# Optimization experiments

Measured on AMD Instinct MI355X. Metric: run time of the kernel, lower is better.

## Reference

```python
import jax, jax.numpy as jnp
import numpy as np

N = 100000
E = 500000
HID = 256
N_EDGE_TYPES = 5
N_ATOM = 16
N_CHARGE = 7
NUM_RBF = 16
CUTOFF = 5.0
LN_EPS = 1e-5


def _xavier(key, shape):
    fan_in, fan_out = shape[0], shape[1]
    lim = float(np.sqrt(6.0 / (fan_in + fan_out)))
    return jax.random.uniform(key, shape, jnp.float32, -lim, lim)


def setup_inputs() -> dict:
    key = jax.random.key(0)
    ks = jax.random.split(key, 12)
    input_dim = HID * 2 + NUM_RBF + N_ATOM + N_CHARGE  # 551
    h = jax.random.normal(ks[0], (N, HID), jnp.float32)
    x = jax.random.normal(ks[1], (N, 3), jnp.float32)
    spawn_node_idx = jax.random.randint(ks[2], (E,), 0, N)
    existing_node_idx = jax.random.randint(ks[3], (E,), 0, N)
    ins_x = jax.random.normal(ks[4], (E, 3), jnp.float32)
    ins_a = jax.random.randint(ks[5], (E,), 0, N_ATOM)
    ins_c = jax.random.randint(ks[6], (E,), 0, N_CHARGE)
    # MLP params (Xavier weights, zero biases; LayerNorm gamma=1, beta=0)
    W1 = _xavier(ks[7], (input_dim, HID)); b1 = jnp.zeros((HID,), jnp.float32)
    g1 = jnp.ones((HID,), jnp.float32); be1 = jnp.zeros((HID,), jnp.float32)
    W2 = _xavier(ks[8], (HID, HID // 2)); b2 = jnp.zeros((HID // 2,), jnp.float32)
    g2 = jnp.ones((HID // 2,), jnp.float32); be2 = jnp.zeros((HID // 2,), jnp.float32)
    W3 = _xavier(ks[9], (HID // 2, N_EDGE_TYPES)); b3 = jnp.zeros((N_EDGE_TYPES,), jnp.float32)
    # Gaussian RBF parameters: centers on [0, cutoff], shared width from spacing
    rbf_mu = jnp.linspace(0.0, CUTOFF, NUM_RBF).astype(jnp.float32)
    delta = CUTOFF / (NUM_RBF - 1)
    rbf_gamma = jnp.asarray(1.0 / (2.0 * delta * delta), jnp.float32)
    return {"h": h, "x": x, "spawn_node_idx": spawn_node_idx,
            "existing_node_idx": existing_node_idx, "ins_x": ins_x,
            "ins_a": ins_a, "ins_c": ins_c,
            "W1": W1, "b1": b1, "g1": g1, "be1": be1,
            "W2": W2, "b2": b2, "g2": g2, "be2": be2,
            "W3": W3, "b3": b3, "rbf_mu": rbf_mu, "rbf_gamma": rbf_gamma}


def _layer_norm(z, gamma, beta):
    mu = jnp.mean(z, axis=-1, keepdims=True)
    var = jnp.mean((z - mu) ** 2, axis=-1, keepdims=True)
    return (z - mu) * jax.lax.rsqrt(var + LN_EPS) * gamma + beta


def reference(h, x, spawn_node_idx, existing_node_idx, ins_x, ins_a, ins_c,
              W1, b1, g1, be1, W2, b2, g2, be2, W3, b3, rbf_mu, rbf_gamma):
    # gather node pairs  [E, HID] / [E, 3]
    h_spawn = h[spawn_node_idx]
    h_existing = h[existing_node_idx]
    existing_pos = x[existing_node_idx]
    # distance + Gaussian RBF  [E, NUM_RBF]
    d = jnp.maximum(jnp.linalg.norm(ins_x - existing_pos, axis=-1), 1e-6)
    dist_features = jnp.exp(-rbf_gamma * (d[:, None] - rbf_mu) ** 2)
    # one-hot insertion type features
    ins_atom = jax.nn.one_hot(ins_a, N_ATOM, dtype=h.dtype)
    ins_charge = jax.nn.one_hot(ins_c, N_CHARGE, dtype=h.dtype)
    feats = jnp.concatenate([h_spawn, h_existing, dist_features, ins_atom, ins_charge], axis=-1)
    # 3-layer MLP: Linear -> LN -> SiLU -> Linear -> LN -> SiLU -> Linear
    z = jax.nn.silu(_layer_norm(feats @ W1 + b1, g1, be1))
    z = jax.nn.silu(_layer_norm(z @ W2 + b2, g2, be2))
    return z @ W3 + b3  # [E, N_EDGE_TYPES]
```

## Files before the change

### kernel.cpp

```cpp
#include <hip/hip_runtime.h>
#include <stdint.h>

#define NN 100000
#define EE 500000
#define HIDD 256
#define LN_EPS 1e-5f

typedef _Float16 half8 __attribute__((ext_vector_type(8)));
typedef _Float16 half4 __attribute__((ext_vector_type(4)));
typedef __fp16 fp16x2 __attribute__((ext_vector_type(2)));
typedef float f32x4 __attribute__((ext_vector_type(4)));

#define LBAR() asm volatile("s_waitcnt lgkmcnt(0)\n\ts_barrier" ::: "memory")

__device__ __forceinline__ unsigned short f2h(float f) {
  _Float16 h = (_Float16)f;
  union { _Float16 hh; unsigned short us; } u; u.hh = h;
  return u.us;
}

__device__ __forceinline__ unsigned pkrtz(float a, float b) {
  union { fp16x2 h; unsigned u; } c;
  c.h = __builtin_amdgcn_cvt_pkrtz(a, b);
  return c.u;
}

__device__ __forceinline__ float fast_silu(float y) {
  float e = __expf(-y);
  return y * __builtin_amdgcn_rcpf(1.f + e);
}

__device__ __forceinline__ half8 ldg8(const unsigned short* p) {
  return *(const half8*)p;
}

__global__ __launch_bounds__(256) void prep_kern(const float* __restrict__ h,
                                                 const float* __restrict__ W1,
                                                 const float* __restrict__ W2,
                                                 const float* __restrict__ W3,
                                                 unsigned short* __restrict__ hb,
                                                 unsigned short* __restrict__ w1sw,
                                                 unsigned short* __restrict__ w2sw,
                                                 unsigned short* __restrict__ w3sw) {
  int b = blockIdx.x;
  if (b < 712) {
    int t = b * 256 + threadIdx.x;
    if (t < 147456) {
      int chunk = t >> 14, rem = t & 16383;
      int kq = rem >> 11, n = (rem >> 3) & 255, j = rem & 7;
      int k = (chunk << 6) + (kq << 3) + j;
      float v = (k < 551) ? W1[k * 256 + n] : 0.f;
      w1sw[t] = f2h(v);
    } else if (t < 147456 + 32768) {
      int t2 = t - 147456;
      int chunk = t2 >> 13, rem = t2 & 8191;
      int kq = rem >> 10, n = (rem >> 3) & 127, j = rem & 7;
      int k = (chunk << 6) + (kq << 3) + j;
      w2sw[t2] = f2h(W2[k * 128 + n]);
    } else if (t < 147456 + 32768 + 2048) {
      int t3 = t - 180224;
      int kq = t3 >> 7, o = (t3 >> 3) & 15, j = t3 & 7;
      int k = (kq << 3) + j;
      w3sw[t3] = f2h((o < 5) ? W3[k * 5 + o] : 0.f);
    }
  } else {
    int i = ((b - 712) * 256 + threadIdx.x) * 8;
    float4 v0 = *(const float4*)(h + i);
    float4 v1 = *(const float4*)(h + i + 4);
    uint4 u;
    u.x = pkrtz(v0.x, v0.y); u.y = pkrtz(v0.z, v0.w);
    u.z = pkrtz(v1.x, v1.y); u.w = pkrtz(v1.z, v1.w);
    *(uint4*)(hb + i) = u;
  }
}

struct __align__(16) SMem {
  short r1[16384];
  float red[512];
  _Float16 b1h[256], g1h[256], be1h[256];
  _Float16 b2h[128], g2h[128], be2h[128];
  float muv[16];
  float b3v[8];
  int spI[64], exI[64];
};

__global__ __launch_bounds__(256, 3)
void edge_head_main(const float* __restrict__ h, const float* __restrict__ x,
                    const int* __restrict__ spawn, const int* __restrict__ exist,
                    const float* __restrict__ insx, const int* __restrict__ insa,
                    const int* __restrict__ insc,
                    const float* __restrict__ b1, const float* __restrict__ g1,
                    const float* __restrict__ be1,
                    const float* __restrict__ b2, const float* __restrict__ g2,
                    const float* __restrict__ be2,
                    const float* __restrict__ b3, const float* __restrict__ mu,
                    const float* __restrict__ gammaP,
                    const unsigned short* __restrict__ w1sw,
                    const unsigned short* __restrict__ w2sw,
                    const unsigned short* __restrict__ w3swg,
                    const unsigned short* __restrict__ hb, int use_hb,
                    float* __restrict__ out) {
  __shared__ SMem sm;
  const int t = threadIdx.x;
  const int base = blockIdx.x * 64;
  const int lane = t & 63;
  const int wv = t >> 6;
  const int cl = lane & 15;
  const int q = lane >> 4;
  const int sx = (cl & 7) << 3;

  sm.b1h[t] = (_Float16)b1[t]; sm.g1h[t] = (_Float16)g1[t]; sm.be1h[t] = (_Float16)be1[t];
  if (t < 128) { sm.b2h[t] = (_Float16)b2[t]; sm.g2h[t] = (_Float16)g2[t]; sm.be2h[t] = (_Float16)be2[t]; }
  if (t < 16) sm.muv[t] = mu[t];
  if (t < 8) sm.b3v[t] = (t < 5) ? b3[t] : 0.f;
  if (t < 64) {
    int e = base + t; int ec = e < EE ? e : EE - 1;
    sm.spI[t] = spawn[ec]; sm.exI[t] = exist[ec];
  }
  const float gma = gammaP[0];

  LBAR();

  int4 f8a = {0,0,0,0}, f8b = {0,0,0,0};
  int k1 = 16, k2 = 32;
  if (t < 64) {
    int e = base + t; int ec = e < EE ? e : EE - 1;
    float ix0 = insx[ec * 3], ix1 = insx[ec * 3 + 1], ix2 = insx[ec * 3 + 2];
    int nd = sm.exI[t];
    float dx = ix0 - x[nd * 3], dy = ix1 - x[nd * 3 + 1], dz = ix2 - x[nd * 3 + 2];
    float d = fmaxf(sqrtf(dx * dx + dy * dy + dz * dz), 1e-6f);
    k1 = 16 + insa[ec]; k2 = 32 + insc[ec];
    float rb[16];
#pragma unroll
    for (int k = 0; k < 16; ++k) { float dd = d - sm.muv[k]; rb[k] = __expf(-gma * dd * dd); }
    uint4 ua, ub;
    ua.x = pkrtz(rb[0], rb[1]);  ua.y = pkrtz(rb[2], rb[3]);
    ua.z = pkrtz(rb[4], rb[5]);  ua.w = pkrtz(rb[6], rb[7]);
    ub.x = pkrtz(rb[8], rb[9]);  ub.y = pkrtz(rb[10], rb[11]);
    ub.z = pkrtz(rb[12], rb[13]); ub.w = pkrtz(rb[14], rb[15]);
    f8a = *(int4*)&ua; f8b = *(int4*)&ub;
  }

  const int row0 = t >> 3, p0 = t & 7;
  const int row1 = row0 + 32;
  const int sw0 = ((p0 ^ (row0 & 7)) << 3);
  const int sw1 = ((p0 ^ (row1 & 7)) << 3);

  int4 pA, pB;
  if (use_hb) {
    pA = *(const int4*)(hb + (size_t)sm.spI[row0] * HIDD + p0 * 8);
    pB = *(const int4*)(hb + (size_t)sm.spI[row1] * HIDD + p0 * 8);
  } else {
    const float* sA = h + (size_t)sm.spI[row0] * HIDD + p0 * 8;
    const float* sB = h + (size_t)sm.spI[row1] * HIDD + p0 * 8;
    float4 a0 = *(const float4*)sA, a1 = *(const float4*)(sA + 4);
    float4 b0 = *(const float4*)sB, b1v_ = *(const float4*)(sB + 4);
    uint4 ua, ub;
    ua.x = pkrtz(a0.x, a0.y); ua.y = pkrtz(a0.z, a0.w); ua.z = pkrtz(a1.x, a1.y); ua.w = pkrtz(a1.z, a1.w);
    ub.x = pkrtz(b0.x, b0.y); ub.y = pkrtz(b0.z, b0.w); ub.z = pkrtz(b1v_.x, b1v_.y); ub.w = pkrtz(b1v_.z, b1v_.w);
    pA = *(int4*)&ua; pB = *(int4*)&ub;
  }
  *(int4*)&sm.r1[row0 * 64 + sw0] = pA;
  *(int4*)&sm.r1[row1 * 64 + sw1] = pB;
  if (use_hb) {
    pA = *(const int4*)(hb + (size_t)sm.spI[row0] * HIDD + 64 + p0 * 8);
    pB = *(const int4*)(hb + (size_t)sm.spI[row1] * HIDD + 64 + p0 * 8);
  } else {
    const float* sA = h + (size_t)sm.spI[row0] * HIDD + 64 + p0 * 8;
    const float* sB = h + (size_t)sm.spI[row1] * HIDD + 64 + p0 * 8;
    float4 a0 = *(const float4*)sA, a1 = *(const float4*)(sA + 4);
    float4 b0 = *(const float4*)sB, b1v_ = *(const float4*)(sB + 4);
    uint4 ua, ub;
    ua.x = pkrtz(a0.x, a0.y); ua.y = pkrtz(a0.z, a0.w); ua.z = pkrtz(a1.x, a1.y); ua.w = pkrtz(a1.z, a1.w);
    ub.x = pkrtz(b0.x, b0.y); ub.y = pkrtz(b0.z, b0.w); ub.z = pkrtz(b1v_.x, b1v_.y); ub.w = pkrtz(b1v_.z, b1v_.w);
    pA = *(int4*)&ua; pB = *(int4*)&ub;
  }

  const unsigned short* w1p = w1sw + q * 2048 + wv * 512 + cl * 8;
  half8 fcur[8], fnext[8];
#pragma unroll
  for (int ks = 0; ks < 2; ++ks)
#pragma unroll
    for (int i = 0; i < 4; ++i)
      fcur[ks * 4 + i] = ldg8(w1p + ks * 8192 + i * 128);

  LBAR();

  f32x4 acc[4][4];
#pragma unroll
  for (int i = 0; i < 4; ++i)
#pragma unroll
    for (int j = 0; j < 4; ++j) acc[i][j] = (f32x4){0.f, 0.f, 0.f, 0.f};

#pragma unroll
  for (int c = 0; c < 9; ++c) {
    if (c < 7) {
      const int nb = ((c + 1) & 1) * 4096;
      *(int4*)&sm.r1[nb + row0 * 64 + sw0] = pA;
      *(int4*)&sm.r1[nb + row1 * 64 + sw1] = pB;
      if (c < 6) {
        const int cn = c + 2;
        const int* sel = (cn < 4) ? sm.spI : sm.exI;
        const int colb = (cn & 3) * 64;
        if (use_hb) {
          pA = *(const int4*)(hb + (size_t)sel[row0] * HIDD + colb + p0 * 8);
          pB = *(const int4*)(hb + (size_t)sel[row1] * HIDD + colb + p0 * 8);
        } else {
          const float* sA = h + (size_t)sel[row0] * HIDD + colb + p0 * 8;
          const float* sB = h + (size_t)sel[row1] * HIDD + colb + p0 * 8;
          float4 a0 = *(const float4*)sA, a1 = *(const float4*)(sA + 4);
          float4 b0 = *(const float4*)sB, b1v_ = *(const float4*)(sB + 4);
          uint4 ua, ub;
          ua.x = pkrtz(a0.x, a0.y); ua.y = pkrtz(a0.z, a0.w); ua.z = pkrtz(a1.x, a1.y); ua.w = pkrtz(a1.z, a1.w);
          ub.x = pkrtz(b0.x, b0.y); ub.y = pkrtz(b0.z, b0.w); ub.z = pkrtz(b1v_.x, b1v_.y); ub.w = pkrtz(b1v_.z, b1v_.w);
          pA = *(int4*)&ua; pB = *(int4*)&ub;
        }
      }
    } else if (c == 7) {
      if (t < 64) {
        short* rp = &sm.r1[t * 64];
        const int sw = t & 7;
#pragma unroll
        for (int g = 0; g < 8; ++g) {
          int4 v = (g == 0) ? f8a : (g == 1) ? f8b : (int4){0, 0, 0, 0};
          *(int4*)&rp[(g ^ sw) * 8] = v;
        }
        rp[((k1 >> 3) ^ sw) * 8 + (k1 & 7)] = (short)0x3C00;
        rp[((k2 >> 3) ^ sw) * 8 + (k2 & 7)] = (short)0x3C00;
      }
    }
    if (c < 8) {
      const unsigned short* wp = w1p + (c + 1) * 16384;
#pragma unroll
      for (int ks = 0; ks < 2; ++ks)
#pragma unroll
        for (int i = 0; i < 4; ++i)
          fnext[ks * 4 + i] = ldg8(wp + ks * 8192 + i * 128);
    }
    const int cb = (c & 1) * 4096;
#pragma unroll
    for (int ks = 0; ks < 2; ++ks) {
      half8 bf[4];
#pragma unroll
      for (int j = 0; j < 4; ++j)
        bf[j] = *(const half8*)&sm.r1[cb + (j * 16 + cl) * 64 + ((ks * 32 + q * 8) ^ sx)];
#pragma unroll
      for (int i = 0; i < 4; ++i)
#pragma unroll
        for (int j = 0; j < 4; ++j)
          acc[i][j] = __builtin_amdgcn_mfma_f32_16x16x32_f16(fcur[ks * 4 + i], bf[j], acc[i][j], 0, 0, 0);
    }
#pragma unroll
    for (int u = 0; u < 8; ++u) fcur[u] = fnext[u];
    LBAR();
  }

  float bf1[4][4];
#pragma unroll
  for (int i = 0; i < 4; ++i) {
    half4 b4 = *(const half4*)&sm.b1h[wv * 64 + i * 16 + q * 4];
#pragma unroll
    for (int r = 0; r < 4; ++r) bf1[i][r] = (float)b4[r];
  }
  float S1arr[4], Q1arr[4];
#pragma unroll
  for (int j = 0; j < 4; ++j) {
    float S = 0.f, Q = 0.f;
#pragma unroll
    for (int i = 0; i < 4; ++i)
#pragma unroll
      for (int r = 0; r < 4; ++r) {
        float v = acc[i][j][r] + bf1[i][r];
        acc[i][j][r] = v; S += v; Q += v * v;
      }
    S += __shfl_xor(S, 16); S += __shfl_xor(S, 32);
    Q += __shfl_xor(Q, 16); Q += __shfl_xor(Q, 32);
    S1arr[j] = S; Q1arr[j] = Q;
  }
  if (q == 0) {
#pragma unroll
    for (int j = 0; j < 4; ++j) {
      sm.red[wv * 64 + j * 16 + cl] = S1arr[j];
      sm.red[256 + wv * 64 + j * 16 + cl] = Q1arr[j];
    }
  }
  LBAR();
  float mean1[4], rstd1[4];
#pragma unroll
  for (int j = 0; j < 4; ++j) {
    int m = j * 16 + cl;
    float S = sm.red[m] + sm.red[64 + m] + sm.red[128 + m] + sm.red[192 + m];
    float Q = sm.red[256 + m] + sm.red[320 + m] + sm.red[384 + m] + sm.red[448 + m];
    float mn = S * (1.f / 256.f);
    mean1[j] = mn;
    rstd1[j] = rsqrtf(Q * (1.f / 256.f) - mn * mn + LN_EPS);
  }
#pragma unroll
  for (int i = 0; i < 4; ++i) {
    half4 g4 = *(const half4*)&sm.g1h[wv * 64 + i * 16 + q * 4];
    half4 e4 = *(const half4*)&sm.be1h[wv * 64 + i * 16 + q * 4];
    float gf[4], ef[4];
#pragma unroll
    for (int r = 0; r < 4; ++r) { gf[r] = (float)g4[r]; ef[r] = (float)e4[r]; }
#pragma unroll
    for (int j = 0; j < 4; ++j) {
      float s0 = fast_silu((acc[i][j][0] - mean1[j]) * rstd1[j] * gf[0] + ef[0]);
      float s1 = fast_silu((acc[i][j][1] - mean1[j]) * rstd1[j] * gf[1] + ef[1]);
      float s2 = fast_silu((acc[i][j][2] - mean1[j]) * rstd1[j] * gf[2] + ef[2]);
      float s3 = fast_silu((acc[i][j][3] - mean1[j]) * rstd1[j] * gf[3] + ef[3]);
      uint2 w; w.x = pkrtz(s0, s1); w.y = pkrtz(s2, s3);
      int m = j * 16 + cl;
      int k0 = wv * 64 + i * 16 + q * 4;
      *(uint2*)&sm.r1[m * 256 + (k0 ^ ((m & 7) << 3))] = w;
    }
  }
  LBAR();

  half8 af3[4];
#pragma unroll
  for (int ks = 0; ks < 4; ++ks)
    af3[ks] = ldg8(w3swg + (ks * 4 + q) * 128 + cl * 8);

  const unsigned short* w2p = w2sw + q * 1024 + wv * 256 + cl * 8;
  f32x4 acc2[2][4];
#pragma unroll
  for (int i = 0; i < 2; ++i)
#pragma unroll
    for (int j = 0; j < 4; ++j) acc2[i][j] = (f32x4){0.f, 0.f, 0.f, 0.f};
#pragma unroll
  for (int c2 = 0; c2 < 4; ++c2) {
#pragma unroll
    for (int ks = 0; ks < 2; ++ks) {
      half8 a0 = ldg8(w2p + c2 * 8192 + ks * 4096);
      half8 a1 = ldg8(w2p + c2 * 8192 + ks * 4096 + 128);
      half8 bf[4];
#pragma unroll
      for (int j = 0; j < 4; ++j)
        bf[j] = *(const half8*)&sm.r1[(j * 16 + cl) * 256 + ((c2 * 64 + ks * 32 + q * 8) ^ sx)];
#pragma unroll
      for (int j = 0; j < 4; ++j) {
        acc2[0][j] = __builtin_amdgcn_mfma_f32_16x16x32_f16(a0, bf[j], acc2[0][j], 0, 0, 0);
        acc2[1][j] = __builtin_amdgcn_mfma_f32_16x16x32_f16(a1, bf[j], acc2[1][j], 0, 0, 0);
      }
    }
  }

  float bf2[2][4];
#pragma unroll
  for (int i = 0; i < 2; ++i) {
    half4 b4 = *(const half4*)&sm.b2h[wv * 32 + i * 16 + q * 4];
#pragma unroll
    for (int r = 0; r < 4; ++r) bf2[i][r] = (float)b4[r];
  }
  float S2arr[4], Q2arr[4];
#pragma unroll
  for (int j = 0; j < 4; ++j) {
    float S = 0.f, Q = 0.f;
#pragma unroll
    for (int i = 0; i < 2; ++i)
#pragma unroll
      for (int r = 0; r < 4; ++r) {
        float v = acc2[i][j][r] + bf2[i][r];
        acc2[i][j][r] = v; S += v; Q += v * v;
      }
    S += __shfl_xor(S, 16); S += __shfl_xor(S, 32);
    Q += __shfl_xor(Q, 16); Q += __shfl_xor(Q, 32);
    S2arr[j] = S; Q2arr[j] = Q;
  }
  if (q == 0) {
#pragma unroll
    for (int j = 0; j < 4; ++j) {
      sm.red[wv * 64 + j * 16 + cl] = S2arr[j];
      sm.red[256 + wv * 64 + j * 16 + cl] = Q2arr[j];
    }
  }
  LBAR();
  float mean2[4], rstd2[4];
#pragma unroll
  for (int j = 0; j < 4; ++j) {
    int m = j * 16 + cl;
    float S = sm.red[m] + sm.red[64 + m] + sm.red[128 + m] + sm.red[192 + m];
    float Q = sm.red[256 + m] + sm.red[320 + m] + sm.red[384 + m] + sm.red[448 + m];
    float mn = S * (1.f / 128.f);
    mean2[j] = mn;
    rstd2[j] = rsqrtf(Q * (1.f / 128.f) - mn * mn + LN_EPS);
  }
#pragma unroll
  for (int i = 0; i < 2; ++i) {
    half4 g4 = *(const half4*)&sm.g2h[wv * 32 + i * 16 + q * 4];
    half4 e4 = *(const half4*)&sm.be2h[wv * 32 + i * 16 + q * 4];
    float gf[4], ef[4];
#pragma unroll
    for (int r = 0; r < 4; ++r) { gf[r] = (float)g4[r]; ef[r] = (float)e4[r]; }
#pragma unroll
    for (int j = 0; j < 4; ++j) {
      float s0 = fast_silu((acc2[i][j][0] - mean2[j]) * rstd2[j] * gf[0] + ef[0]);
      float s1 = fast_silu((acc2[i][j][1] - mean2[j]) * rstd2[j] * gf[1] + ef[1]);
      float s2 = fast_silu((acc2[i][j][2] - mean2[j]) * rstd2[j] * gf[2] + ef[2]);
      float s3 = fast_silu((acc2[i][j][3] - mean2[j]) * rstd2[j] * gf[3] + ef[3]);
      uint2 w; w.x = pkrtz(s0, s1); w.y = pkrtz(s2, s3);
      int m = j * 16 + cl;
      int k0 = wv * 32 + i * 16 + q * 4;
      *(uint2*)&sm.r1[m * 128 + (k0 ^ ((m & 7) << 3))] = w;
    }
  }
  LBAR();

  f32x4 a3 = (f32x4){0.f, 0.f, 0.f, 0.f};
  const int m3 = wv * 16 + cl;
  const int sx3 = (m3 & 7) << 3;
#pragma unroll
  for (int ks = 0; ks < 4; ++ks) {
    half8 bf = *(const half8*)&sm.r1[m3 * 128 + ((ks * 32 + q * 8) ^ sx3)];
    a3 = __builtin_amdgcn_mfma_f32_16x16x32_f16(af3[ks], bf, a3, 0, 0, 0);
  }
  int e = base + m3;
  if (e < EE) {
#pragma unroll
    for (int r = 0; r < 4; ++r) {
      int o = q * 4 + r;
      if (o < 5) out[e * 5 + o] = a3[r] + sm.b3v[o];
    }
  }
}

extern "C" void kernel_launch(void* const* d_in, const int* in_sizes, int n_in,
                              void* d_out, int out_size, void* d_ws, size_t ws_size,
                              hipStream_t stream) {
  const float* h    = (const float*)d_in[0];
  const float* x    = (const float*)d_in[1];
  const int* spawn  = (const int*)d_in[2];
  const int* exist  = (const int*)d_in[3];
  const float* insx = (const float*)d_in[4];
  const int* insa   = (const int*)d_in[5];
  const int* insc   = (const int*)d_in[6];
  const float* W1   = (const float*)d_in[7];
  const float* b1   = (const float*)d_in[8];
  const float* g1   = (const float*)d_in[9];
  const float* be1  = (const float*)d_in[10];
  const float* W2   = (const float*)d_in[11];
  const float* b2   = (const float*)d_in[12];
  const float* g2   = (const float*)d_in[13];
  const float* be2  = (const float*)d_in[14];
  const float* W3   = (const float*)d_in[15];
  const float* b3   = (const float*)d_in[16];
  const float* mu   = (const float*)d_in[17];
  const float* gma  = (const float*)d_in[18];

  unsigned short* w1sw = (unsigned short*)d_ws;
  unsigned short* w2sw = w1sw + 147456;
  unsigned short* w3sw = w2sw + 32768;
  unsigned short* hb   = w3sw + 2048;
  const size_t need_hb = 364544ull + (size_t)NN * HIDD * 2ull;
  int use_hb = (ws_size >= need_hb) ? 1 : 0;

  prep_kern<<<use_hb ? 13212 : 712, 256, 0, stream>>>(h, W1, W2, W3, hb, w1sw, w2sw, w3sw);
  edge_head_main<<<7813, 256, 0, stream>>>(h, x, spawn, exist, insx, insa, insc,
                                           b1, g1, be1, b2, g2, be2, b3, mu, gma,
                                           w1sw, w2sw, w3sw, hb, use_hb,
                                           (float*)d_out);
}
```

Baseline: 426.1 us.

## Cut register pressure in edge MLP kernel and raise occupancy to four blocks

Raises the launch-bounds occupancy target from 3 to 4 blocks per SIMD. To fit that register budget, it splits W1 fragment prefetch into two half-sets reloaded right after use, and defers the RBF computation so only the distance stays live. It also uses packed float2 math for the bias and LayerNorm epilogues and stages outputs through shared memory for coalesced float4 stores. The risk is spilling or shorter prefetch distance exposing global-load latency for the W1 fragments.

```diff
diff --git a/kernel.cpp b/kernel.cpp
--- a/kernel.cpp
+++ b/kernel.cpp
@@ -10,6 +10,7 @@
 typedef _Float16 half4 __attribute__((ext_vector_type(4)));
 typedef __fp16 fp16x2 __attribute__((ext_vector_type(2)));
 typedef float f32x4 __attribute__((ext_vector_type(4)));
+typedef float f32x2 __attribute__((ext_vector_type(2)));
 
 #define LBAR() asm volatile("s_waitcnt lgkmcnt(0)\n\ts_barrier" ::: "memory")
 
@@ -32,6 +33,14 @@
 
 __device__ __forceinline__ half8 ldg8(const unsigned short* p) {
   return *(const half8*)p;
+}
+
+__device__ __forceinline__ int4 cvt_row(const float* s) {
+  float4 a0 = *(const float4*)s, a1 = *(const float4*)(s + 4);
+  uint4 ua;
+  ua.x = pkrtz(a0.x, a0.y); ua.y = pkrtz(a0.z, a0.w);
+  ua.z = pkrtz(a1.x, a1.y); ua.w = pkrtz(a1.z, a1.w);
+  return *(int4*)&ua;
 }
 
 __global__ __launch_bounds__(256) void prep_kern(const float* __restrict__ h,
@@ -84,7 +93,7 @@
   int spI[64], exI[64];
 };
 
-__global__ __launch_bounds__(256, 3)
+__global__ __launch_bounds__(256, 4)
 void edge_head_main(const float* __restrict__ h, const float* __restrict__ x,
                     const int* __restrict__ spawn, const int* __restrict__ exist,
                     const float* __restrict__ insx, const int* __restrict__ insa,
@@ -121,24 +130,15 @@
 
   LBAR();
 
-  int4 f8a = {0,0,0,0}, f8b = {0,0,0,0};
+  float dreg = 0.f;
   int k1 = 16, k2 = 32;
   if (t < 64) {
     int e = base + t; int ec = e < EE ? e : EE - 1;
     float ix0 = insx[ec * 3], ix1 = insx[ec * 3 + 1], ix2 = insx[ec * 3 + 2];
     int nd = sm.exI[t];
     float dx = ix0 - x[nd * 3], dy = ix1 - x[nd * 3 + 1], dz = ix2 - x[nd * 3 + 2];
-    float d = fmaxf(sqrtf(dx * dx + dy * dy + dz * dz), 1e-6f);
+    dreg = fmaxf(sqrtf(dx * dx + dy * dy + dz * dz), 1e-6f);
     k1 = 16 + insa[ec]; k2 = 32 + insc[ec];
-    float rb[16];
-#pragma unroll
-    for (int k = 0; k < 16; ++k) { float dd = d - sm.muv[k]; rb[k] = __expf(-gma * dd * dd); }
-    uint4 ua, ub;
-    ua.x = pkrtz(rb[0], rb[1]);  ua.y = pkrtz(rb[2], rb[3]);
-    ua.z = pkrtz(rb[4], rb[5]);  ua.w = pkrtz(rb[6], rb[7]);
-    ub.x = pkrtz(rb[8], rb[9]);  ub.y = pkrtz(rb[10], rb[11]);
-    ub.z = pkrtz(rb[12], rb[13]); ub.w = pkrtz(rb[14], rb[15]);
-    f8a = *(int4*)&ua; f8b = *(int4*)&ub;
   }
 
   const int row0 = t >> 3, p0 = t & 7;
@@ -151,14 +151,8 @@
     pA = *(const int4*)(hb + (size_t)sm.spI[row0] * HIDD + p0 * 8);
     pB = *(const int4*)(hb + (size_t)sm.spI[row1] * HIDD + p0 * 8);
   } else {
-    const float* sA = h + (size_t)sm.spI[row0] * HIDD + p0 * 8;
-    const float* sB = h + (size_t)sm.spI[row1] * HIDD + p0 * 8;
-    float4 a0 = *(const float4*)sA, a1 = *(const float4*)(sA + 4);
-    float4 b0 = *(const float4*)sB, b1v_ = *(const float4*)(sB + 4);
-    uint4 ua, ub;
-    ua.x = pkrtz(a0.x, a0.y); ua.y = pkrtz(a0.z, a0.w); ua.z = pkrtz(a1.x, a1.y); ua.w = pkrtz(a1.z, a1.w);
-    ub.x = pkrtz(b0.x, b0.y); ub.y = pkrtz(b0.z, b0.w); ub.z = pkrtz(b1v_.x, b1v_.y); ub.w = pkrtz(b1v_.z, b1v_.w);
-    pA = *(int4*)&ua; pB = *(int4*)&ub;
+    pA = cvt_row(h + (size_t)sm.spI[row0] * HIDD + p0 * 8);
+    pB = cvt_row(h + (size_t)sm.spI[row1] * HIDD + p0 * 8);
   }
   *(int4*)&sm.r1[row0 * 64 + sw0] = pA;
   *(int4*)&sm.r1[row1 * 64 + sw1] = pB;
@@ -166,23 +160,16 @@
     pA = *(const int4*)(hb + (size_t)sm.spI[row0] * HIDD + 64 + p0 * 8);
     pB = *(const int4*)(hb + (size_t)sm.spI[row1] * HIDD + 64 + p0 * 8);
   } else {
-    const float* sA = h + (size_t)sm.spI[row0] * HIDD + 64 + p0 * 8;
-    const float* sB = h + (size_t)sm.spI[row1] * HIDD + 64 + p0 * 8;
-    float4 a0 = *(const float4*)sA, a1 = *(const float4*)(sA + 4);
-    float4 b0 = *(const float4*)sB, b1v_ = *(const float4*)(sB + 4);
-    uint4 ua, ub;
-    ua.x = pkrtz(a0.x, a0.y); ua.y = pkrtz(a0.z, a0.w); ua.z = pkrtz(a1.x, a1.y); ua.w = pkrtz(a1.z, a1.w);
-    ub.x = pkrtz(b0.x, b0.y); ub.y = pkrtz(b0.z, b0.w); ub.z = pkrtz(b1v_.x, b1v_.y); ub.w = pkrtz(b1v_.z, b1v_.w);
-    pA = *(int4*)&ua; pB = *(int4*)&ub;
+    pA = cvt_row(h + (size_t)sm.spI[row0] * HIDD + 64 + p0 * 8);
+    pB = cvt_row(h + (size_t)sm.spI[row1] * HIDD + 64 + p0 * 8);
   }
 
   const unsigned short* w1p = w1sw + q * 2048 + wv * 512 + cl * 8;
-  half8 fcur[8], fnext[8];
-#pragma unroll
-  for (int ks = 0; ks < 2; ++ks)
-#pragma unroll
-    for (int i = 0; i < 4; ++i)
-      fcur[ks * 4 + i] = ldg8(w1p + ks * 8192 + i * 128);
+  half8 fA[4], fB[4];
+#pragma unroll
+  for (int i = 0; i < 4; ++i) fA[i] = ldg8(w1p + i * 128);
+#pragma unroll
+  for (int i = 0; i < 4; ++i) fB[i] = ldg8(w1p + 8192 + i * 128);
 
   LBAR();
 
@@ -206,73 +193,89 @@
           pA = *(const int4*)(hb + (size_t)sel[row0] * HIDD + colb + p0 * 8);
           pB = *(const int4*)(hb + (size_t)sel[row1] * HIDD + colb + p0 * 8);
         } else {
-          const float* sA = h + (size_t)sel[row0] * HIDD + colb + p0 * 8;
-          const float* sB = h + (size_t)sel[row1] * HIDD + colb + p0 * 8;
-          float4 a0 = *(const float4*)sA, a1 = *(const float4*)(sA + 4);
-          float4 b0 = *(const float4*)sB, b1v_ = *(const float4*)(sB + 4);
-          uint4 ua, ub;
-          ua.x = pkrtz(a0.x, a0.y); ua.y = pkrtz(a0.z, a0.w); ua.z = pkrtz(a1.x, a1.y); ua.w = pkrtz(a1.z, a1.w);
-          ub.x = pkrtz(b0.x, b0.y); ub.y = pkrtz(b0.z, b0.w); ub.z = pkrtz(b1v_.x, b1v_.y); ub.w = pkrtz(b1v_.z, b1v_.w);
-          pA = *(int4*)&ua; pB = *(int4*)&ub;
+          pA = cvt_row(h + (size_t)sel[row0] * HIDD + colb + p0 * 8);
+          pB = cvt_row(h + (size_t)sel[row1] * HIDD + colb + p0 * 8);
         }
       }
     } else if (c == 7) {
       if (t < 64) {
         short* rp = &sm.r1[t * 64];
         const int sw = t & 7;
-#pragma unroll
-        for (int g = 0; g < 8; ++g) {
-          int4 v = (g == 0) ? f8a : (g == 1) ? f8b : (int4){0, 0, 0, 0};
-          *(int4*)&rp[(g ^ sw) * 8] = v;
-        }
+        float rb[16];
+#pragma unroll
+        for (int k = 0; k < 16; ++k) { float dd = dreg - sm.muv[k]; rb[k] = __expf(-gma * dd * dd); }
+        uint4 ua, ub;
+        ua.x = pkrtz(rb[0], rb[1]);  ua.y = pkrtz(rb[2], rb[3]);
+        ua.z = pkrtz(rb[4], rb[5]);  ua.w = pkrtz(rb[6], rb[7]);
+        ub.x = pkrtz(rb[8], rb[9]);  ub.y = pkrtz(rb[10], rb[11]);
+        ub.z = pkrtz(rb[12], rb[13]); ub.w = pkrtz(rb[14], rb[15]);
+        *(int4*)&rp[(0 ^ sw) * 8] = *(int4*)&ua;
+        *(int4*)&rp[(1 ^ sw) * 8] = *(int4*)&ub;
+        const int4 z4 = {0, 0, 0, 0};
+#pragma unroll
+        for (int g = 2; g < 8; ++g) *(int4*)&rp[(g ^ sw) * 8] = z4;
         rp[((k1 >> 3) ^ sw) * 8 + (k1 & 7)] = (short)0x3C00;
         rp[((k2 >> 3) ^ sw) * 8 + (k2 & 7)] = (short)0x3C00;
       }
     }
+    const int cb = (c & 1) * 4096;
+    {
+      half8 bf[4];
+#pragma unroll
+      for (int j = 0; j < 4; ++j)
+        bf[j] = *(const half8*)&sm.r1[cb + (j * 16 + cl) * 64 + ((q * 8) ^ sx)];
+#pragma unroll
+      for (int i = 0; i < 4; ++i)
+#pragma unroll
+        for (int j = 0; j < 4; ++j)
+          acc[i][j] = __builtin_amdgcn_mfma_f32_16x16x32_f16(fA[i], bf[j], acc[i][j], 0, 0, 0);
+    }
     if (c < 8) {
       const unsigned short* wp = w1p + (c + 1) * 16384;
 #pragma unroll
-      for (int ks = 0; ks < 2; ++ks)
-#pragma unroll
-        for (int i = 0; i < 4; ++i)
-          fnext[ks * 4 + i] = ldg8(wp + ks * 8192 + i * 128);
-    }
-    const int cb = (c & 1) * 4096;
-#pragma unroll
-    for (int ks = 0; ks < 2; ++ks) {
+      for (int i = 0; i < 4; ++i) fA[i] = ldg8(wp + i * 128);
+    }
+    {
       half8 bf[4];
 #pragma unroll
       for (int j = 0; j < 4; ++j)
-        bf[j] = *(const half8*)&sm.r1[cb + (j * 16 + cl) * 64 + ((ks * 32 + q * 8) ^ sx)];
+        bf[j] = *(const half8*)&sm.r1[cb + (j * 16 + cl) * 64 + ((32 + q * 8) ^ sx)];
 #pragma unroll
       for (int i = 0; i < 4; ++i)
 #pragma unroll
         for (int j = 0; j < 4; ++j)
-          acc[i][j] = __builtin_amdgcn_mfma_f32_16x16x32_f16(fcur[ks * 4 + i], bf[j], acc[i][j], 0, 0, 0);
-    }
-#pragma unroll
-    for (int u = 0; u < 8; ++u) fcur[u] = fnext[u];
+          acc[i][j] = __builtin_amdgcn_mfma_f32_16x16x32_f16(fB[i], bf[j], acc[i][j], 0, 0, 0);
+    }
+    if (c < 8) {
+      const unsigned short* wp = w1p + (c + 1) * 16384 + 8192;
+#pragma unroll
+      for (int i = 0; i < 4; ++i) fB[i] = ldg8(wp + i * 128);
+    }
     LBAR();
   }
 
-  float bf1[4][4];
+  f32x2 bb1[4][2];
 #pragma unroll
   for (int i = 0; i < 4; ++i) {
     half4 b4 = *(const half4*)&sm.b1h[wv * 64 + i * 16 + q * 4];
-#pragma unroll
-    for (int r = 0; r < 4; ++r) bf1[i][r] = (float)b4[r];
+    bb1[i][0] = (f32x2){(float)b4[0], (float)b4[1]};
+    bb1[i][1] = (f32x2){(float)b4[2], (float)b4[3]};
   }
   float S1arr[4], Q1arr[4];
 #pragma unroll
   for (int j = 0; j < 4; ++j) {
-    float S = 0.f, Q = 0.f;
-#pragma unroll
-    for (int i = 0; i < 4; ++i)
-#pragma unroll
-      for (int r = 0; r < 4; ++r) {
-        float v = acc[i][j][r] + bf1[i][r];
-        acc[i][j][r] = v; S += v; Q += v * v;
-      }
+    f32x2 S2 = (f32x2){0.f, 0.f}, Q2 = (f32x2){0.f, 0.f};
+#pragma unroll
+    for (int i = 0; i < 4; ++i) {
+      f32x2 v0 = (f32x2){acc[i][j][0], acc[i][j][1]} + bb1[i][0];
+      f32x2 v1 = (f32x2){acc[i][j][2], acc[i][j][3]} + bb1[i][1];
+      acc[i][j][0] = v0[0]; acc[i][j][1] = v0[1];
+      acc[i][j][2] = v1[0]; acc[i][j][3] = v1[1];
+      S2 += v0 + v1;
+      Q2 += v0 * v0;
+      Q2 += v1 * v1;
+    }
+    float S = S2[0] + S2[1], Q = Q2[0] + Q2[1];
     S += __shfl_xor(S, 16); S += __shfl_xor(S, 32);
     Q += __shfl_xor(Q, 16); Q += __shfl_xor(Q, 32);
     S1arr[j] = S; Q1arr[j] = Q;
@@ -285,29 +288,33 @@
     }
   }
   LBAR();
-  float mean1[4], rstd1[4];
+  f32x2 rs1[4], mr1[4];
 #pragma unroll
   for (int j = 0; j < 4; ++j) {
     int m = j * 16 + cl;
     float S = sm.red[m] + sm.red[64 + m] + sm.red[128 + m] + sm.red[192 + m];
     float Q = sm.red[256 + m] + sm.red[320 + m] + sm.red[384 + m] + sm.red[448 + m];
     float mn = S * (1.f / 256.f);
-    mean1[j] = mn;
-    rstd1[j] = rsqrtf(Q * (1.f / 256.f) - mn * mn + LN_EPS);
+    float rs = rsqrtf(Q * (1.f / 256.f) - mn * mn + LN_EPS);
+    rs1[j] = (f32x2){rs, rs};
+    mr1[j] = (f32x2){-mn * rs, -mn * rs};
   }
 #pragma unroll
   for (int i = 0; i < 4; ++i) {
     half4 g4 = *(const half4*)&sm.g1h[wv * 64 + i * 16 + q * 4];
     half4 e4 = *(const half4*)&sm.be1h[wv * 64 + i * 16 + q * 4];
-    float gf[4], ef[4];
-#pragma unroll
-    for (int r = 0; r < 4; ++r) { gf[r] = (float)g4[r]; ef[r] = (float)e4[r]; }
+    f32x2 gg0 = (f32x2){(float)g4[0], (float)g4[1]}, gg1 = (f32x2){(float)g4[2], (float)g4[3]};
+    f32x2 ee0 = (f32x2){(float)e4[0], (float)e4[1]}, ee1 = (f32x2){(float)e4[2], (float)e4[3]};
 #pragma unroll
     for (int j = 0; j < 4; ++j) {
-      float s0 = fast_silu((acc[i][j][0] - mean1[j]) * rstd1[j] * gf[0] + ef[0]);
-      float s1 = fast_silu((acc[i][j][1] - mean1[j]) * rstd1[j] * gf[1] + ef[1]);
-      float s2 = fast_silu((acc[i][j][2] - mean1[j]) * rstd1[j] * gf[2] + ef[2]);
-      float s3 = fast_silu((acc[i][j][3] - mean1[j]) * rstd1[j] * gf[3] + ef[3]);
+      f32x2 v0 = (f32x2){acc[i][j][0], acc[i][j][1]};
+      f32x2 v1 = (f32x2){acc[i][j][2], acc[i][j][3]};
+      f32x2 t0 = v0 * rs1[j] + mr1[j];
+      f32x2 t1 = v1 * rs1[j] + mr1[j];
+      f32x2 y0 = t0 * gg0 + ee0;
+      f32x2 y1 = t1 * gg1 + ee1;
+      float s0 = fast_silu(y0[0]), s1 = fast_silu(y0[1]);
+      float s2 = fast_silu(y1[0]), s3 = fast_silu(y1[1]);
       uint2 w; w.x = pkrtz(s0, s1); w.y = pkrtz(s2, s3);
       int m = j * 16 + cl;
       int k0 = wv * 64 + i * 16 + q * 4;
@@ -345,24 +352,28 @@
     }
   }
 
-  float bf2[2][4];
+  f32x2 bb2[2][2];
 #pragma unroll
   for (int i = 0; i < 2; ++i) {
     half4 b4 = *(const half4*)&sm.b2h[wv * 32 + i * 16 + q * 4];
-#pragma unroll
-    for (int r = 0; r < 4; ++r) bf2[i][r] = (float)b4[r];
+    bb2[i][0] = (f32x2){(float)b4[0], (float)b4[1]};
+    bb2[i][1] = (f32x2){(float)b4[2], (float)b4[3]};
   }
   float S2arr[4], Q2arr[4];
 #pragma unroll
   for (int j = 0; j < 4; ++j) {
-    float S = 0.f, Q = 0.f;
-#pragma unroll
-    for (int i = 0; i < 2; ++i)
-#pragma unroll
-      for (int r = 0; r < 4; ++r) {
-        float v = acc2[i][j][r] + bf2[i][r];
-        acc2[i][j][r] = v; S += v; Q += v * v;
-      }
+    f32x2 S2 = (f32x2){0.f, 0.f}, Q2 = (f32x2){0.f, 0.f};
+#pragma unroll
+    for (int i = 0; i < 2; ++i) {
+      f32x2 v0 = (f32x2){acc2[i][j][0], acc2[i][j][1]} + bb2[i][0];
+      f32x2 v1 = (f32x2){acc2[i][j][2], acc2[i][j][3]} + bb2[i][1];
+      acc2[i][j][0] = v0[0]; acc2[i][j][1] = v0[1];
+      acc2[i][j][2] = v1[0]; acc2[i][j][3] = v1[1];
+      S2 += v0 + v1;
+      Q2 += v0 * v0;
+      Q2 += v1 * v1;
+    }
+    float S = S2[0] + S2[1], Q = Q2[0] + Q2[1];
     S += __shfl_xor(S, 16); S += __shfl_xor(S, 32);
     Q += __shfl_xor(Q, 16); Q += __shfl_xor(Q, 32);
     S2arr[j] = S; Q2arr[j] = Q;
@@ -375,29 +386,33 @@
     }
   }
   LBAR();
-  float mean2[4], rstd2[4];
+  f32x2 rs2[4], mr2[4];
 #pragma unroll
   for (int j = 0; j < 4; ++j) {
     int m = j * 16 + cl;
     float S = sm.red[m] + sm.red[64 + m] + sm.red[128 + m] + sm.red[192 + m];
     float Q = sm.red[256 + m] + sm.red[320 + m] + sm.red[384 + m] + sm.red[448 + m];
     float mn = S * (1.f / 128.f);
-    mean2[j] = mn;
-    rstd2[j] = rsqrtf(Q * (1.f / 128.f) - mn * mn + LN_EPS);
+    float rs = rsqrtf(Q * (1.f / 128.f) - mn * mn + LN_EPS);
+    rs2[j] = (f32x2){rs, rs};
+    mr2[j] = (f32x2){-mn * rs, -mn * rs};
   }
 #pragma unroll
   for (int i = 0; i < 2; ++i) {
     half4 g4 = *(const half4*)&sm.g2h[wv * 32 + i * 16 + q * 4];
     half4 e4 = *(const half4*)&sm.be2h[wv * 32 + i * 16 + q * 4];
-    float gf[4], ef[4];
-#pragma unroll
-    for (int r = 0; r < 4; ++r) { gf[r] = (float)g4[r]; ef[r] = (float)e4[r]; }
+    f32x2 gg0 = (f32x2){(float)g4[0], (float)g4[1]}, gg1 = (f32x2){(float)g4[2], (float)g4[3]};
+    f32x2 ee0 = (f32x2){(float)e4[0], (float)e4[1]}, ee1 = (f32x2){(float)e4[2], (float)e4[3]};
 #pragma unroll
     for (int j = 0; j < 4; ++j) {
-      float s0 = fast_silu((acc2[i][j][0] - mean2[j]) * rstd2[j] * gf[0] + ef[0]);
-      float s1 = fast_silu((acc2[i][j][1] - mean2[j]) * rstd2[j] * gf[1] + ef[1]);
-      float s2 = fast_silu((acc2[i][j][2] - mean2[j]) * rstd2[j] * gf[2] + ef[2]);
-      float s3 = fast_silu((acc2[i][j][3] - mean2[j]) * rstd2[j] * gf[3] + ef[3]);
+      f32x2 v0 = (f32x2){acc2[i][j][0], acc2[i][j][1]};
+      f32x2 v1 = (f32x2){acc2[i][j][2], acc2[i][j][3]};
+      f32x2 t0 = v0 * rs2[j] + mr2[j];
+      f32x2 t1 = v1 * rs2[j] + mr2[j];
+      f32x2 y0 = t0 * gg0 + ee0;
+      f32x2 y1 = t1 * gg1 + ee1;
+      float s0 = fast_silu(y0[0]), s1 = fast_silu(y0[1]);
+      float s2 = fast_silu(y1[0]), s3 = fast_silu(y1[1]);
       uint2 w; w.x = pkrtz(s0, s1); w.y = pkrtz(s2, s3);
       int m = j * 16 + cl;
       int k0 = wv * 32 + i * 16 + q * 4;
@@ -411,15 +426,23 @@
   const int sx3 = (m3 & 7) << 3;
 #pragma unroll
   for (int ks = 0; ks < 4; ++ks) {
-    half8 bf = *(const half8*)&sm.r1[m3 * 128 + ((ks * 32 + q * 8) ^ sx3)];
-    a3 = __builtin_amdgcn_mfma_f32_16x16x32_f16(af3[ks], bf, a3, 0, 0, 0);
-  }
-  int e = base + m3;
-  if (e < EE) {
-#pragma unroll
-    for (int r = 0; r < 4; ++r) {
-      int o = q * 4 + r;
-      if (o < 5) out[e * 5 + o] = a3[r] + sm.b3v[o];
+    half8 bfv = *(const half8*)&sm.r1[m3 * 128 + ((ks * 32 + q * 8) ^ sx3)];
+    a3 = __builtin_amdgcn_mfma_f32_16x16x32_f16(af3[ks], bfv, a3, 0, 0, 0);
+  }
+#pragma unroll
+  for (int r = 0; r < 4; ++r) {
+    int o = q * 4 + r;
+    if (o < 5) sm.red[m3 * 5 + o] = a3[r] + sm.b3v[o];
+  }
+  LBAR();
+  if (t < 80) {
+    size_t g = (size_t)base * 5 + (size_t)t * 4;
+    if (g + 4 <= (size_t)EE * 5) {
+      *(float4*)(out + g) = *(const float4*)&sm.red[t * 4];
+    } else {
+#pragma unroll
+      for (int u = 0; u < 4; ++u)
+        if (g + u < (size_t)EE * 5) out[g + u] = sm.red[t * 4 + u];
     }
   }
 }
```

Result: slower. 617.4 us (+44.9%).
